# Kernel optimization log

Measured on AMD Instinct MI355X. Metric: run time of the kernel, lower is better.

Reference implementation:

```python
import jax, jax.numpy as jnp
import numpy as np

B, L, D, H, DH = 2, 2048, 1024, 16, 64
THETA_T = 100.0
EPS_COS = 1e-6
EPS_NORM = 1e-6


def make_rope_tables(n_heads=H, d_head=DH, theta_t=THETA_T):
    dr = d_head // 12                      # 5 rotary freqs per head per axis
    n = n_heads * dr
    log_min, log_max = np.log(np.pi), np.log(10.0 * np.pi)
    f = np.exp(np.linspace(log_min, log_max, n + 1)[:-1])
    freqs = np.stack([f, f]).reshape(2, dr, n_heads).transpose(0, 2, 1)   # (2, H, dr)
    t_freqs = (theta_t ** (-np.arange(n, dtype=np.float64) / n)).reshape(dr, n_heads).T  # (H, dr)
    return jnp.asarray(freqs, jnp.float32), jnp.asarray(t_freqs, jnp.float32)


def rms_norm(x, scale, eps=EPS_NORM):
    ms = jnp.mean(x.astype(jnp.float32) ** 2, axis=-1, keepdims=True)
    return x * (scale.astype(jnp.float32) * jax.lax.rsqrt(ms + eps)).astype(x.dtype)


def rope_theta(pos, pos_orig, time, freqs, t_freqs):
    # pos_to_use: (b, l, c=2, xy=2), mapped to [-1, 1]
    pos_use = jnp.stack([pos_orig, pos], axis=2) * 2.0 - 1.0
    theta_w = pos_use[..., 0][:, :, :, None, None] * freqs[0]      # b l 2 H dr
    theta_h = pos_use[..., 1][:, :, :, None, None] * freqs[1]      # b l 2 H dr
    theta_t = time[:, :, None, None, None] * t_freqs               # b l 1 H dr
    theta = jnp.concatenate([theta_h, theta_w, theta_t], axis=2)   # b l 5 H dr
    b, l = theta.shape[0], theta.shape[1]
    theta = jnp.transpose(theta, (0, 1, 3, 2, 4)).reshape(b, l, H, -1)  # b l H (5*dr)
    return theta


def apply_rotary_emb(x, theta):
    d = theta.shape[-1]
    x1, x2, x3 = x[..., :d], x[..., d:2 * d], x[..., 2 * d:]
    cos, sin = jnp.cos(theta), jnp.sin(theta)
    y1 = x1 * cos - x2 * sin
    y2 = x2 * cos + x1 * sin
    return jnp.concatenate([y1, y2, x3], axis=-1)


def scale_for_cosine_sim(q, k, scale, eps=EPS_COS):
    sq = jnp.sum(q * q, axis=-1, keepdims=True)
    sk = jnp.sum(k * k, axis=-1, keepdims=True)
    sqrt_scale = jnp.sqrt(scale)                         # (H,1,1) -> broadcasts to (b,H,l,1)
    return q * (sqrt_scale * jax.lax.rsqrt(sq + eps)), k * (sqrt_scale * jax.lax.rsqrt(sk + eps))


def setup_inputs() -> dict:
    key = jax.random.key(0)
    ks = jax.random.split(key, 8)
    return {
        "x": jax.random.normal(ks[0], (B, L, D), jnp.float32),
        "pos": jax.random.uniform(ks[1], (B, L, 2), jnp.float32),
        "pos_orig": jax.random.uniform(ks[2], (B, L, 2), jnp.float32),
        "time": jax.random.uniform(ks[3], (B, L), jnp.float32),
        "w_qkv": jax.random.normal(ks[4], (3 * D, D), jnp.float32) * (D ** -0.5),
        "w_out": jax.random.normal(ks[5], (D, D), jnp.float32) * (D ** -0.5),
        "w_up": jax.random.normal(ks[6], (4 * D, D), jnp.float32) * (D ** -0.5),
        "w_down": jax.random.normal(ks[7], (D, 4 * D), jnp.float32) * ((4 * D) ** -0.5),
        "norm1_scale": jnp.ones((D,), jnp.float32),
        "norm2_scale": jnp.ones((D,), jnp.float32),
        "qk_scale": jnp.full((H, 1, 1), 10.0, jnp.float32),
    }


def reference(x, pos, pos_orig, time, w_qkv, w_out, w_up, w_down,
              norm1_scale, norm2_scale, qk_scale):
    freqs, t_freqs = make_rope_tables()
    b, l, _ = x.shape

    # --- attention block (pre-norm) ---
    xn = rms_norm(x, norm1_scale)
    qkv = jnp.einsum('bld,ed->ble', xn, w_qkv)                  # b l 3D
    q, k, v = jnp.split(qkv, 3, axis=-1)
    q = q.reshape(b, l, H, DH)
    k = k.reshape(b, l, H, DH)
    v = v.reshape(b, l, H, DH).transpose(0, 2, 1, 3)            # b H l dh

    theta = rope_theta(pos, pos_orig, time, freqs, t_freqs)      # b l H 25
    q = apply_rotary_emb(q, theta).transpose(0, 2, 1, 3)         # b H l dh
    k = apply_rotary_emb(k, theta).transpose(0, 2, 1, 3)

    q, k = scale_for_cosine_sim(q, k, qk_scale)                  # cosine-sim QK norm
    scores = jnp.einsum('bhqd,bhkd->bhqk', q, k)                 # scale=1 (already folded in)
    probs = jax.nn.softmax(scores, axis=-1)
    attn = jnp.einsum('bhqk,bhkd->bhqd', probs, v)
    attn = attn.transpose(0, 2, 1, 3).reshape(b, l, D)
    x = x + jnp.einsum('bld,ed->ble', attn, w_out)

    h = rms_norm(x, norm2_scale)
    h = jax.nn.gelu(jnp.einsum('bld,ed->ble', h, w_up), approximate=True)
    x = x + jnp.einsum('ble,de->bld', h, w_down)
    return x
```

## Files before the change

kernel.cpp:

```cpp
#include <hip/hip_runtime.h>

#define B_ 2
#define L_ 2048
#define D_ 1024
#define H_ 16
#define DH_ 64

typedef float f32x4 __attribute__((ext_vector_type(4)));
typedef __bf16 bf16x8 __attribute__((ext_vector_type(8)));

__device__ __forceinline__ ushort f2bf(float f) {
  unsigned u = __float_as_uint(f);
  u += 0x7fffu + ((u >> 16) & 1u);
  return (ushort)(u >> 16);
}
__device__ __forceinline__ float bf2f(ushort h) {
  return __uint_as_float(((unsigned)h) << 16);
}

__device__ __forceinline__ void gload_lds16(const void* g, void* l) {
  __builtin_amdgcn_global_load_lds(
      (const __attribute__((address_space(1))) unsigned*)g,
      (__attribute__((address_space(3))) unsigned*)l, 16, 0, 0);
}

__device__ __forceinline__ float gelu_f(float v) {
  return 0.5f * v * (1.0f + tanhf(0.7978845608f * (v + 0.044715f * v * v * v)));
}

__global__ __launch_bounds__(256) void cast_all_kernel(const float* __restrict__ w0,
                                                       const float* __restrict__ w1,
                                                       const float* __restrict__ w2,
                                                       const float* __restrict__ w3,
                                                       ushort* __restrict__ o0,
                                                       ushort* __restrict__ o1,
                                                       ushort* __restrict__ o2,
                                                       ushort* __restrict__ o3) {
  int i = blockIdx.x * 256 + threadIdx.x;
  const float* src;
  ushort* dst;
  int j = i;
  if (j < 786432) { src = w0; dst = o0; }
  else if (j < 786432 + 262144) { j -= 786432; src = w1; dst = o1; }
  else if (j < 786432 + 262144 + 1048576) { j -= 786432 + 262144; src = w2; dst = o2; }
  else { j -= 786432 + 262144 + 1048576; src = w3; dst = o3; }
  float4 v = ((const float4*)src)[j];
  ushort4 o;
  o.x = f2bf(v.x); o.y = f2bf(v.y); o.z = f2bf(v.z); o.w = f2bf(v.w);
  ((ushort4*)dst)[j] = o;
}

template <typename T>
__global__ __launch_bounds__(256) void rmsnorm_kernel(const T* __restrict__ x,
                                                      const float* __restrict__ scale,
                                                      ushort* __restrict__ out) {
  int row = blockIdx.x, t = threadIdx.x;
  float4 v;
  if constexpr (sizeof(T) == 4) {
    v = ((const float4*)((const float*)x + (size_t)row * D_))[t];
  } else {
    ushort4 u = ((const ushort4*)((const ushort*)x + (size_t)row * D_))[t];
    v.x = bf2f(u.x); v.y = bf2f(u.y); v.z = bf2f(u.z); v.w = bf2f(u.w);
  }
  float ss = v.x * v.x + v.y * v.y + v.z * v.z + v.w * v.w;
#pragma unroll
  for (int d = 1; d < 64; d <<= 1) ss += __shfl_xor(ss, d);
  __shared__ float wsum[4];
  if ((t & 63) == 0) wsum[t >> 6] = ss;
  __syncthreads();
  float tot = wsum[0] + wsum[1] + wsum[2] + wsum[3];
  float r = rsqrtf(tot * (1.0f / D_) + 1e-6f);
  float4 sc = ((const float4*)scale)[t];
  ushort4 o;
  o.x = f2bf(v.x * sc.x * r); o.y = f2bf(v.y * sc.y * r);
  o.z = f2bf(v.z * sc.z * r); o.w = f2bf(v.w * sc.w * r);
  ((ushort4*)(out + (size_t)row * D_))[t] = o;
}

template <int EPI, int XR, int XC>
__global__ __launch_bounds__(512, 2) void gemm256(const ushort* __restrict__ A,
                                                  const ushort* __restrict__ Bw,
                                                  void* __restrict__ Cout,
                                                  int M, int N, int K) {
  __shared__ __align__(16) ushort Als[2][2][128 * 64];
  __shared__ __align__(16) ushort Bls[2][2][128 * 64];
  const int tid = threadIdx.x;
  const int lane = tid & 63;
  const int w = tid >> 6;
  const int wm = w >> 2, wn = w & 3;
  const int fr = lane & 15, fg = lane >> 4;
  const int bid = blockIdx.y * gridDim.x + blockIdx.x;
  const int xcd = bid & 7, i0 = bid >> 3;
  const int CR = gridDim.x / XR, CC = gridDim.y / XC;
  const int rt = (xcd % XR) * CR + (i0 % CR);
  const int ct = (xcd / XR) * CC + (i0 / CR);
  const int row0 = rt * 256, col0 = ct * 256;
  const ushort* Ab = A + (size_t)row0 * K;
  const ushort* Bb = Bw + (size_t)col0 * K;
  const int srow = tid >> 3;
  const int sxor = ((tid & 7) ^ (srow & 7)) * 8;

  f32x4 acc[8][4];
  f32x4 zero = {0.f, 0.f, 0.f, 0.f};
#pragma unroll
  for (int m = 0; m < 8; m++)
#pragma unroll
    for (int n = 0; n < 4; n++) acc[m][n] = zero;

  auto stageA = [&](int buf, int half, int kt) {
#pragma unroll
    for (int i = 0; i < 2; i++)
      gload_lds16(Ab + (size_t)(half * 128 + i * 64 + srow) * K + kt + sxor,
                  &Als[buf][half][i * 4096 + tid * 8]);
  };
  auto stageB = [&](int buf, int half, int kt) {
#pragma unroll
    for (int i = 0; i < 2; i++)
      gload_lds16(Bb + (size_t)(half * 128 + i * 64 + srow) * K + kt + sxor,
                  &Bls[buf][half][i * 4096 + tid * 8]);
  };
  const int nt = K >> 6;
  stageA(0, 0, 0); stageB(0, 0, 0); stageB(0, 1, 0); stageA(0, 1, 0);
  asm volatile("s_waitcnt vmcnt(0)" ::: "memory");
  __builtin_amdgcn_s_barrier();

  bf16x8 afr[4][2], b0[2][2], b1[2][2];
  for (int t = 0; t < nt; t++) {
    const int cur = t & 1, nxt = cur ^ 1;
    const int kn = (t + 1) << 6;
    const bool more = (t + 1 < nt);
#pragma unroll
    for (int mf = 0; mf < 4; mf++)
#pragma unroll
      for (int ks = 0; ks < 2; ks++) {
        int r = wm * 64 + mf * 16 + fr;
        afr[mf][ks] = *(const bf16x8*)&Als[cur][0][r * 64 + (((ks * 4 + fg) ^ (r & 7)) << 3)];
      }
#pragma unroll
    for (int nf = 0; nf < 2; nf++)
#pragma unroll
      for (int ks = 0; ks < 2; ks++) {
        int c = wn * 32 + nf * 16 + fr;
        b0[nf][ks] = *(const bf16x8*)&Bls[cur][0][c * 64 + (((ks * 4 + fg) ^ (c & 7)) << 3)];
      }
    if (more) stageA(nxt, 0, kn);
    asm volatile("s_waitcnt vmcnt(4)" ::: "memory");
    __builtin_amdgcn_s_barrier();
    asm volatile("s_waitcnt lgkmcnt(0)" ::: "memory");
    __builtin_amdgcn_sched_barrier(0);
    __builtin_amdgcn_s_setprio(1);
#pragma unroll
    for (int mf = 0; mf < 4; mf++)
#pragma unroll
      for (int nf = 0; nf < 2; nf++)
#pragma unroll
        for (int ks = 0; ks < 2; ks++)
          acc[mf][nf] =
              __builtin_amdgcn_mfma_f32_16x16x32_bf16(afr[mf][ks], b0[nf][ks], acc[mf][nf], 0, 0, 0);
    __builtin_amdgcn_s_setprio(0);
    __builtin_amdgcn_s_barrier();
#pragma unroll
    for (int nf = 0; nf < 2; nf++)
#pragma unroll
      for (int ks = 0; ks < 2; ks++) {
        int c = wn * 32 + nf * 16 + fr;
        b1[nf][ks] = *(const bf16x8*)&Bls[cur][1][c * 64 + (((ks * 4 + fg) ^ (c & 7)) << 3)];
      }
    if (more) stageB(nxt, 0, kn);
    asm volatile("s_waitcnt vmcnt(4)" ::: "memory");
    __builtin_amdgcn_s_barrier();
    asm volatile("s_waitcnt lgkmcnt(0)" ::: "memory");
    __builtin_amdgcn_sched_barrier(0);
    __builtin_amdgcn_s_setprio(1);
#pragma unroll
    for (int mf = 0; mf < 4; mf++)
#pragma unroll
      for (int nf = 0; nf < 2; nf++)
#pragma unroll
        for (int ks = 0; ks < 2; ks++)
          acc[mf][2 + nf] =
              __builtin_amdgcn_mfma_f32_16x16x32_bf16(afr[mf][ks], b1[nf][ks], acc[mf][2 + nf], 0, 0, 0);
    __builtin_amdgcn_s_setprio(0);
    __builtin_amdgcn_s_barrier();
#pragma unroll
    for (int mf = 0; mf < 4; mf++)
#pragma unroll
      for (int ks = 0; ks < 2; ks++) {
        int r = wm * 64 + mf * 16 + fr;
        afr[mf][ks] = *(const bf16x8*)&Als[cur][1][r * 64 + (((ks * 4 + fg) ^ (r & 7)) << 3)];
      }
    if (more) stageB(nxt, 1, kn);
    asm volatile("s_waitcnt vmcnt(4)" ::: "memory");
    __builtin_amdgcn_s_barrier();
    asm volatile("s_waitcnt lgkmcnt(0)" ::: "memory");
    __builtin_amdgcn_sched_barrier(0);
    __builtin_amdgcn_s_setprio(1);
#pragma unroll
    for (int mf = 0; mf < 4; mf++)
#pragma unroll
      for (int nf = 0; nf < 2; nf++)
#pragma unroll
        for (int ks = 0; ks < 2; ks++)
          acc[4 + mf][2 + nf] =
              __builtin_amdgcn_mfma_f32_16x16x32_bf16(afr[mf][ks], b1[nf][ks], acc[4 + mf][2 + nf], 0, 0, 0);
    __builtin_amdgcn_s_setprio(0);
    __builtin_amdgcn_s_barrier();
    if (more) stageA(nxt, 1, kn);
    asm volatile("s_waitcnt vmcnt(4)" ::: "memory");
    __builtin_amdgcn_s_barrier();
    asm volatile("s_waitcnt lgkmcnt(0)" ::: "memory");
    __builtin_amdgcn_sched_barrier(0);
    __builtin_amdgcn_s_setprio(1);
#pragma unroll
    for (int mf = 0; mf < 4; mf++)
#pragma unroll
      for (int nf = 0; nf < 2; nf++)
#pragma unroll
        for (int ks = 0; ks < 2; ks++)
          acc[4 + mf][nf] =
              __builtin_amdgcn_mfma_f32_16x16x32_bf16(afr[mf][ks], b0[nf][ks], acc[4 + mf][nf], 0, 0, 0);
    __builtin_amdgcn_s_setprio(0);
    __builtin_amdgcn_s_barrier();
  }
  const int orow = row0 + wm * 64 + fg * 4;
  const int ocol = col0 + wn * 32 + fr;
#pragma unroll
  for (int am = 0; am < 8; am++) {
#pragma unroll
    for (int j = 0; j < 4; j++) {
      int r = orow + (am >> 2) * 128 + (am & 3) * 16 + j;
#pragma unroll
      for (int an = 0; an < 4; an++) {
        int cidx = ocol + (an >> 1) * 128 + (an & 1) * 16;
        size_t idx = (size_t)r * N + cidx;
        float v = acc[am][an][j];
        if (EPI == 0) {
          ((ushort*)Cout)[idx] = f2bf(v);
        } else {
          ((ushort*)Cout)[idx] = f2bf(gelu_f(v));
        }
      }
    }
  }
}

template <int EPI, int BM, int BN, int DEPTH, int XR, int XC, bool CTFAST>
__global__ __launch_bounds__(256) void gemm_nt(const ushort* __restrict__ A,
                                               const ushort* __restrict__ Bw,
                                               void* __restrict__ Cout,
                                               const void* __restrict__ resid,
                                               int M, int N, int K, int Klen) {
  constexpr int WROWS = BM / 2, WCOLS = BN / 2;
  constexpr int MR = WROWS / 16, NR = WCOLS / 16;
  constexpr int ALOADS = BM / 64, BLOADS = BN / 64;
  constexpr int NLOADS = ALOADS + BLOADS;
  __shared__ __align__(16) ushort Als[DEPTH][BM * 32];
  __shared__ __align__(16) ushort Bls[DEPTH][BN * 32];
  const int tid = threadIdx.x;
  const int lane = tid & 63;
  const int w = tid >> 6;
  const int wr = w >> 1, wc = w & 1;
  const int bid = blockIdx.y * gridDim.x + blockIdx.x;
  const int xcd = bid & 7;
  const int i0 = bid >> 3;
  const int CR = gridDim.x / XR, CC = gridDim.y / XC;
  int rt, ct;
  if constexpr (CTFAST) {
    rt = (xcd % XR) * CR + (i0 / CC);
    ct = (xcd / XR) * CC + (i0 % CC);
  } else {
    rt = (xcd % XR) * CR + (i0 % CR);
    ct = (xcd / XR) * CC + (i0 / CR);
  }
  const int row0 = rt * BM;
  const int col0 = ct * BN;
  const int koff = blockIdx.z * Klen;
  const ushort* Ab = A + (size_t)row0 * K + koff;
  const ushort* Bb = Bw + (size_t)col0 * K + koff;
  const int sr = tid >> 2;
  const int scA = (((tid & 3) ^ ((tid >> 3) & 3)) * 8);
  const int fr = lane & 15;
  const int fg = lane >> 4;
  f32x4 zero = {0.f, 0.f, 0.f, 0.f};
  f32x4 acc[MR][NR];
#pragma unroll
  for (int m = 0; m < MR; m++)
#pragma unroll
    for (int n = 0; n < NR; n++) acc[m][n] = zero;

  auto stage = [&](int slot, int kt) {
#pragma unroll
    for (int i2 = 0; i2 < ALOADS; i2++)
      gload_lds16(Ab + (size_t)(sr + 64 * i2) * K + kt + scA, &Als[slot][i2 * 2048 + tid * 8]);
#pragma unroll
    for (int i2 = 0; i2 < BLOADS; i2++)
      gload_lds16(Bb + (size_t)(sr + 64 * i2) * K + kt + scA, &Bls[slot][i2 * 2048 + tid * 8]);
  };
  const int nt = Klen >> 5;
#pragma unroll
  for (int p = 0; p < DEPTH - 1; p++) stage(p, p << 5);
  int cur = 0, sbuf = DEPTH - 1;
  for (int t = 0; t < nt; t++) {
    const int ahead = nt - 1 - t;
    if constexpr (DEPTH == 3) {
      if (ahead >= 1) asm volatile("s_waitcnt vmcnt(%0)" ::"i"(NLOADS) : "memory");
      else            asm volatile("s_waitcnt vmcnt(0)" ::: "memory");
    } else if constexpr (DEPTH == 4) {
      if (ahead >= 2)      asm volatile("s_waitcnt vmcnt(%0)" ::"i"(2 * NLOADS) : "memory");
      else if (ahead == 1) asm volatile("s_waitcnt vmcnt(%0)" ::"i"(NLOADS) : "memory");
      else                 asm volatile("s_waitcnt vmcnt(0)" ::: "memory");
    } else {
      if (ahead >= 3)      asm volatile("s_waitcnt vmcnt(%0)" ::"i"(3 * NLOADS) : "memory");
      else if (ahead == 2) asm volatile("s_waitcnt vmcnt(%0)" ::"i"(2 * NLOADS) : "memory");
      else if (ahead == 1) asm volatile("s_waitcnt vmcnt(%0)" ::"i"(NLOADS) : "memory");
      else                 asm volatile("s_waitcnt vmcnt(0)" ::: "memory");
    }
    __builtin_amdgcn_s_barrier();
    if (t + DEPTH - 1 < nt) {
      stage(sbuf, (t + DEPTH - 1) << 5);
      sbuf = (sbuf == DEPTH - 1) ? 0 : sbuf + 1;
    }
    bf16x8 af[MR], bfr[NR];
#pragma unroll
    for (int m = 0; m < MR; m++) {
      int rA = wr * WROWS + m * 16 + fr;
      af[m] = *(const bf16x8*)&Als[cur][rA * 32 + ((fg ^ ((rA >> 1) & 3)) << 3)];
    }
#pragma unroll
    for (int n = 0; n < NR; n++) {
      int rB = wc * WCOLS + n * 16 + fr;
      bfr[n] = *(const bf16x8*)&Bls[cur][rB * 32 + ((fg ^ ((rB >> 1) & 3)) << 3)];
    }
#pragma unroll
    for (int m = 0; m < MR; m++)
#pragma unroll
      for (int n = 0; n < NR; n++)
        acc[m][n] = __builtin_amdgcn_mfma_f32_16x16x32_bf16(af[m], bfr[n], acc[m][n], 0, 0, 0);
    cur = (cur == DEPTH - 1) ? 0 : cur + 1;
  }
  const int orow = row0 + wr * WROWS + fg * 4;
  const int ocol = col0 + wc * WCOLS + fr;
  float* Pz = (float*)Cout + (size_t)blockIdx.z * M * N;
#pragma unroll
  for (int m = 0; m < MR; m++) {
#pragma unroll
    for (int j = 0; j < 4; j++) {
      int r = orow + m * 16 + j;
#pragma unroll
      for (int n = 0; n < NR; n++) {
        int cidx = ocol + n * 16;
        size_t idx = (size_t)r * N + cidx;
        float v = acc[m][n][j];
        if (EPI == 0) {
          ((ushort*)Cout)[idx] = f2bf(v);
        } else if (EPI == 1) {
          ((ushort*)Cout)[idx] = f2bf(((const float*)resid)[idx] + v);
        } else if (EPI == 2) {
          ((ushort*)Cout)[idx] = f2bf(gelu_f(v));
        } else if (EPI == 3) {
          ((float*)Cout)[idx] = bf2f(((const ushort*)resid)[idx]) + v;
        } else {
          Pz[idx] = v;
        }
      }
    }
  }
}

__global__ __launch_bounds__(256) void reduce_down_kernel(const float* __restrict__ P0,
                                                          const float* __restrict__ P1,
                                                          const ushort* __restrict__ residb,
                                                          float* __restrict__ out) {
  int i = blockIdx.x * 256 + threadIdx.x;
  float4 a = ((const float4*)P0)[i];
  float4 b = ((const float4*)P1)[i];
  ushort4 r = ((const ushort4*)residb)[i];
  float4 o;
  o.x = a.x + b.x + bf2f(r.x);
  o.y = a.y + b.y + bf2f(r.y);
  o.z = a.z + b.z + bf2f(r.z);
  o.w = a.w + b.w + bf2f(r.w);
  ((float4*)out)[i] = o;
}

__global__ __launch_bounds__(256) void rope_kernel(const ushort* __restrict__ qkv,
                                                   const float* __restrict__ pos,
                                                   const float* __restrict__ pos_orig,
                                                   const float* __restrict__ timep,
                                                   const float* __restrict__ qk_scale,
                                                   ushort* __restrict__ qr,
                                                   ushort* __restrict__ kr) {
  int gw = (blockIdx.x * 256 + threadIdx.x) >> 6;
  int lane = threadIdx.x & 63;
  int h = gw & 15;
  int row = gw >> 4;
  int b = row >> 11;
  int l = row & (L_ - 1);
  float qv = bf2f(qkv[(size_t)row * 3072 + h * 64 + lane]);
  float kv = bf2f(qkv[(size_t)row * 3072 + 1024 + h * 64 + lane]);
  float c = 1.0f, s = 0.0f;
  if (lane < 50) {
    int idx = lane < 25 ? lane : lane - 25;
    int sg = idx / 5, d = idx % 5;
    int fi = d * 16 + h;
    float th;
    if (sg == 4) {
      th = timep[row] * __expf(-(float)fi * 0.05756462732485115f);
    } else {
      float fr = 3.14159265358979323846f * __expf((float)fi * 0.028782313662425575f);
      const float* psrc = (sg == 0 || sg == 2) ? pos_orig : pos;
      int comp = (sg < 2) ? 1 : 0;
      th = (2.0f * psrc[(size_t)row * 2 + comp] - 1.0f) * fr;
    }
    s = sinf(th);
    c = cosf(th);
  }
  int partner = lane < 25 ? lane + 25 : lane - 25;
  float qp = __shfl(qv, partner, 64);
  float kp = __shfl(kv, partner, 64);
  float yq, yk;
  if (lane < 25) { yq = qv * c - qp * s; yk = kv * c - kp * s; }
  else if (lane < 50) { yq = qv * c + qp * s; yk = kv * c + kp * s; }
  else { yq = qv; yk = kv; }
  float sq = yq * yq, sk = yk * yk;
#pragma unroll
  for (int d = 1; d < 64; d <<= 1) { sq += __shfl_xor(sq, d); sk += __shfl_xor(sk, d); }
  float scl = sqrtf(qk_scale[h]);
  float qo = yq * scl * rsqrtf(sq + 1e-6f);
  float ko = yk * scl * rsqrtf(sk + 1e-6f);
  size_t o = ((size_t)(b * 16 + h) * L_ + l) * 64 + lane;
  qr[o] = f2bf(qo);
  kr[o] = f2bf(ko);
}

__global__ __launch_bounds__(256) void vtrans_kernel(const ushort* __restrict__ qkv,
                                                     ushort* __restrict__ vT) {
  __shared__ __align__(16) ushort tile[64][72];
  int t = threadIdx.x;
  int lt = blockIdx.x;
  int bh = blockIdx.y;
  int b = bh >> 4, h = bh & 15;
  int r = t >> 3, c0 = (t & 7) * 8;
#pragma unroll
  for (int half = 0; half < 2; half++) {
    const ushort* src =
        qkv + (size_t)(b * L_ + lt * 64 + r + half * 32) * 3072 + 2048 + h * 64 + c0;
    *(uint4*)&tile[r + half * 32][c0] = *(const uint4*)src;
  }
  __syncthreads();
#pragma unroll
  for (int half = 0; half < 2; half++) {
    int dh = r + half * 32;
    unsigned p0 = (unsigned)tile[c0 + 0][dh] | ((unsigned)tile[c0 + 1][dh] << 16);
    unsigned p1 = (unsigned)tile[c0 + 2][dh] | ((unsigned)tile[c0 + 3][dh] << 16);
    unsigned p2 = (unsigned)tile[c0 + 4][dh] | ((unsigned)tile[c0 + 5][dh] << 16);
    unsigned p3 = (unsigned)tile[c0 + 6][dh] | ((unsigned)tile[c0 + 7][dh] << 16);
    uint4 o; o.x = p0; o.y = p1; o.z = p2; o.w = p3;
    *(uint4*)&vT[((size_t)bh * 64 + dh) * L_ + lt * 64 + c0] = o;
  }
}

__global__ __launch_bounds__(256) void attn_kernel(const ushort* __restrict__ qr,
                                                   const ushort* __restrict__ kr,
                                                   const ushort* __restrict__ vT,
                                                   ushort* __restrict__ attnb) {
  __shared__ __align__(16) ushort Kls[2][64 * 64];
  __shared__ __align__(16) ushort Vls[2][64 * 64];
  __shared__ __align__(16) ushort Pls[4][2][16 * 64];
  const int tid = threadIdx.x, lane = tid & 63, w = tid >> 6;
  const int bid = blockIdx.x;
  const int qp = (bid >> 3) & 15;
  const int bh = (bid & 7) | ((bid >> 7) << 3);
  const int b = bh >> 4;
  const int fr = lane & 15, fg = lane >> 4;
  const ushort* Qb0 = qr + ((size_t)bh * L_ + qp * 128 + w * 16) * 64;
  const ushort* Qb1 = Qb0 + 64 * 64;
  bf16x8 qf0[2], qf1[2];
#pragma unroll
  for (int c = 0; c < 2; c++) {
    qf0[c] = *(const bf16x8*)(Qb0 + fr * 64 + c * 32 + fg * 8);
    qf1[c] = *(const bf16x8*)(Qb1 + fr * 64 + c * 32 + fg * 8);
  }
  const ushort ob[8] = {0x3F80, 0x3F80, 0x3F80, 0x3F80, 0x3F80, 0x3F80, 0x3F80, 0x3F80};
  const bf16x8 ones = *(const bf16x8*)ob;
  f32x4 zero = {0.f, 0.f, 0.f, 0.f};
  f32x4 accO0[4], accO1[4], acc1_0 = zero, acc1_1 = zero;
#pragma unroll
  for (int n = 0; n < 4; n++) { accO0[n] = zero; accO1[n] = zero; }
  const int sr = tid >> 3;
  const int scz = (((tid & 7) ^ (sr & 7)) * 8);
  auto stage = [&](int buf, int kt) {
    gload_lds16(kr + ((size_t)bh * L_ + kt + sr) * 64 + scz, &Kls[buf][tid * 8]);
    gload_lds16(kr + ((size_t)bh * L_ + kt + 32 + sr) * 64 + scz, &Kls[buf][2048 + tid * 8]);
    gload_lds16(vT + ((size_t)bh * 64 + sr) * L_ + kt + scz, &Vls[buf][tid * 8]);
    gload_lds16(vT + ((size_t)bh * 64 + 32 + sr) * L_ + kt + scz, &Vls[buf][2048 + tid * 8]);
  };
  stage(0, 0);
  int cur = 0;
  for (int t = 0; t < (L_ >> 6); t++) {
    asm volatile("s_waitcnt vmcnt(0)" ::: "memory");
    __builtin_amdgcn_s_barrier();
    __builtin_amdgcn_sched_barrier(0);
    if (t + 1 < (L_ >> 6)) stage(cur ^ 1, (t + 1) << 6);
    f32x4 sv0[4], sv1[4];
#pragma unroll
    for (int n = 0; n < 4; n++) { sv0[n] = zero; sv1[n] = zero; }
    __builtin_amdgcn_s_setprio(1);
#pragma unroll
    for (int c = 0; c < 2; c++) {
#pragma unroll
      for (int n = 0; n < 4; n++) {
        bf16x8 kf =
            *(const bf16x8*)&Kls[cur][(n * 16 + fr) * 64 + (((c * 4 + fg) ^ (fr & 7)) << 3)];
        sv0[n] = __builtin_amdgcn_mfma_f32_16x16x32_bf16(qf0[c], kf, sv0[n], 0, 0, 0);
        sv1[n] = __builtin_amdgcn_mfma_f32_16x16x32_bf16(qf1[c], kf, sv1[n], 0, 0, 0);
      }
    }
    __builtin_amdgcn_s_setprio(0);
#pragma unroll
    for (int qs = 0; qs < 2; qs++) {
      const f32x4* sv = qs ? sv1 : sv0;
#pragma unroll
      for (int j = 0; j < 4; j++) {
        int row = fg * 4 + j;
        int rbase = row * 64;
        int rx = row & 7;
#pragma unroll
        for (int n = 0; n < 4; n++) {
          float p = __builtin_amdgcn_exp2f(
              fmaf(sv[n][j], 1.4426950408889634f, -17.31234049066756f));
          int chunk = 2 * n + (fr >> 3);
          Pls[w][qs][rbase + ((chunk ^ rx) << 3) + (fr & 7)] =
              (ushort)(__float_as_uint(p) >> 16);
        }
      }
    }
    __builtin_amdgcn_s_setprio(1);
#pragma unroll
    for (int c = 0; c < 2; c++) {
      bf16x8 pa0 = *(const bf16x8*)&Pls[w][0][fr * 64 + (((c * 4 + fg) ^ (fr & 7)) << 3)];
      bf16x8 pa1 = *(const bf16x8*)&Pls[w][1][fr * 64 + (((c * 4 + fg) ^ (fr & 7)) << 3)];
#pragma unroll
      for (int n = 0; n < 4; n++) {
        bf16x8 vb =
            *(const bf16x8*)&Vls[cur][(n * 16 + fr) * 64 + (((c * 4 + fg) ^ (fr & 7)) << 3)];
        accO0[n] = __builtin_amdgcn_mfma_f32_16x16x32_bf16(pa0, vb, accO0[n], 0, 0, 0);
        accO1[n] = __builtin_amdgcn_mfma_f32_16x16x32_bf16(pa1, vb, accO1[n], 0, 0, 0);
      }
      acc1_0 = __builtin_amdgcn_mfma_f32_16x16x32_bf16(pa0, ones, acc1_0, 0, 0, 0);
      acc1_1 = __builtin_amdgcn_mfma_f32_16x16x32_bf16(pa1, ones, acc1_1, 0, 0, 0);
    }
    __builtin_amdgcn_s_setprio(0);
    cur ^= 1;
  }
#pragma unroll
  for (int qs = 0; qs < 2; qs++) {
    const f32x4* accO = qs ? accO1 : accO0;
    const f32x4& acc1 = qs ? acc1_1 : acc1_0;
    float inv[4];
#pragma unroll
    for (int j = 0; j < 4; j++) inv[j] = 1.0f / acc1[j];
#pragma unroll
    for (int n = 0; n < 4; n++) {
#pragma unroll
      for (int j = 0; j < 4; j++) {
        float o = accO[n][j] * inv[j];
        int qrow = qp * 128 + qs * 64 + w * 16 + fg * 4 + j;
        int dh = fr + n * 16;
        attnb[(size_t)(b * L_ + qrow) * 1024 + (bh & 15) * 64 + dh] = f2bf(o);
      }
    }
  }
}

extern "C" void kernel_launch(void* const* d_in, const int* in_sizes, int n_in,
                              void* d_out, int out_size, void* d_ws, size_t ws_size,
                              hipStream_t stream) {
  const float* x = (const float*)d_in[0];
  const float* pos = (const float*)d_in[1];
  const float* pos_orig = (const float*)d_in[2];
  const float* timep = (const float*)d_in[3];
  const float* w_qkv = (const float*)d_in[4];
  const float* w_out = (const float*)d_in[5];
  const float* w_up = (const float*)d_in[6];
  const float* w_down = (const float*)d_in[7];
  const float* norm1 = (const float*)d_in[8];
  const float* norm2 = (const float*)d_in[9];
  const float* qk_scale = (const float*)d_in[10];
  float* out = (float*)d_out;
  char* ws = (char*)d_ws;
  size_t off = 0;
  auto alloc = [&](size_t bytes) {
    void* p = ws + off;
    off += bytes;
    return p;
  };
  ushort* xn = (ushort*)alloc(8ull << 20);
  ushort* qkvb = (ushort*)alloc(32ull << 20);
  ushort* qrb = (ushort*)alloc(8ull << 20);
  ushort* krb = (ushort*)alloc(8ull << 20);
  ushort* vTb = (ushort*)alloc(8ull << 20);
  ushort* attnb = (ushort*)alloc(8ull << 20);
  ushort* x1b = (ushort*)alloc(8ull << 20);
  ushort* wqkvb = (ushort*)alloc(6ull << 20);
  ushort* woutb = (ushort*)alloc(2ull << 20);
  ushort* wupb = (ushort*)alloc(8ull << 20);
  ushort* wdownb = (ushort*)alloc(8ull << 20);
  float* Ppart = (float*)qrb;

  cast_all_kernel<<<12288, 256, 0, stream>>>(w_qkv, w_out, w_up, w_down,
                                             wqkvb, woutb, wupb, wdownb);

  rmsnorm_kernel<float><<<4096, 256, 0, stream>>>(x, norm1, xn);
  gemm256<0, 4, 2><<<dim3(16, 12), 512, 0, stream>>>(xn, wqkvb, qkvb, 4096, 3072, 1024);
  rope_kernel<<<16384, 256, 0, stream>>>(qkvb, pos, pos_orig, timep, qk_scale, qrb, krb);
  vtrans_kernel<<<dim3(32, 32), 256, 0, stream>>>(qkvb, vTb);
  attn_kernel<<<512, 256, 0, stream>>>(qrb, krb, vTb, attnb);
  gemm_nt<1, 64, 64, 5, 4, 2, false><<<dim3(64, 16), 256, 0, stream>>>(
      attnb, woutb, x1b, x, 4096, 1024, 1024, 1024);
  rmsnorm_kernel<ushort><<<4096, 256, 0, stream>>>(x1b, norm2, xn);
  gemm256<2, 4, 2><<<dim3(16, 16), 512, 0, stream>>>(xn, wupb, qkvb, 4096, 4096, 1024);
  gemm_nt<4, 128, 128, 4, 4, 2, true><<<dim3(32, 8, 2), 256, 0, stream>>>(
      qkvb, wdownb, Ppart, nullptr, 4096, 1024, 4096, 2048);
  reduce_down_kernel<<<4096, 256, 0, stream>>>(Ppart, Ppart + (4u << 20), x1b, out);
}
```

Baseline: 266.9 us.

## Split attention over two KV halves with a separate combine kernel

The attention kernel now launches twice as many blocks. Each block processes half of the key/value sequence and writes unnormalized fp32 partial outputs and softmax denominators to scratch buffers. A new combine kernel sums the two halves, normalizes, and casts to bf16. The log2(e) factor is folded into the q scaling in the rope kernel, and the constant max offset is dropped, so the inner loop does a bare exp2. The intent is better CU occupancy, at the cost of extra fp32 scratch traffic and another launch.

```diff
diff --git a/kernel.cpp b/kernel.cpp
--- a/kernel.cpp
+++ b/kernel.cpp
@@ -426,7 +426,7 @@
 #pragma unroll
   for (int d = 1; d < 64; d <<= 1) { sq += __shfl_xor(sq, d); sk += __shfl_xor(sk, d); }
   float scl = sqrtf(qk_scale[h]);
-  float qo = yq * scl * rsqrtf(sq + 1e-6f);
+  float qo = yq * (scl * 1.4426950408889634f) * rsqrtf(sq + 1e-6f);
   float ko = yk * scl * rsqrtf(sk + 1e-6f);
   size_t o = ((size_t)(b * 16 + h) * L_ + l) * 64 + lane;
   qr[o] = f2bf(qo);
@@ -463,14 +463,16 @@
 __global__ __launch_bounds__(256) void attn_kernel(const ushort* __restrict__ qr,
                                                    const ushort* __restrict__ kr,
                                                    const ushort* __restrict__ vT,
-                                                   ushort* __restrict__ attnb) {
+                                                   float* __restrict__ po,
+                                                   float* __restrict__ den) {
   __shared__ __align__(16) ushort Kls[2][64 * 64];
   __shared__ __align__(16) ushort Vls[2][64 * 64];
   __shared__ __align__(16) ushort Pls[4][2][16 * 64];
   const int tid = threadIdx.x, lane = tid & 63, w = tid >> 6;
   const int bid = blockIdx.x;
-  const int qp = (bid >> 3) & 15;
-  const int bh = (bid & 7) | ((bid >> 7) << 3);
+  const int kvh = (bid >> 3) & 1;
+  const int qp = (bid >> 4) & 15;
+  const int bh = (bid & 7) | ((bid >> 8) << 3);
   const int b = bh >> 4;
   const int fr = lane & 15, fg = lane >> 4;
   const ushort* Qb0 = qr + ((size_t)bh * L_ + qp * 128 + w * 16) * 64;
@@ -495,13 +497,14 @@
     gload_lds16(vT + ((size_t)bh * 64 + sr) * L_ + kt + scz, &Vls[buf][tid * 8]);
     gload_lds16(vT + ((size_t)bh * 64 + 32 + sr) * L_ + kt + scz, &Vls[buf][2048 + tid * 8]);
   };
-  stage(0, 0);
+  const int t0 = kvh << 4;
+  stage(0, t0 << 6);
   int cur = 0;
-  for (int t = 0; t < (L_ >> 6); t++) {
+  for (int t = t0; t < t0 + 16; t++) {
     asm volatile("s_waitcnt vmcnt(0)" ::: "memory");
     __builtin_amdgcn_s_barrier();
     __builtin_amdgcn_sched_barrier(0);
-    if (t + 1 < (L_ >> 6)) stage(cur ^ 1, (t + 1) << 6);
+    if (t + 1 < t0 + 16) stage(cur ^ 1, (t + 1) << 6);
     f32x4 sv0[4], sv1[4];
 #pragma unroll
     for (int n = 0; n < 4; n++) { sv0[n] = zero; sv1[n] = zero; }
@@ -527,8 +530,7 @@
         int rx = row & 7;
 #pragma unroll
         for (int n = 0; n < 4; n++) {
-          float p = __builtin_amdgcn_exp2f(
-              fmaf(sv[n][j], 1.4426950408889634f, -17.31234049066756f));
+          float p = __builtin_amdgcn_exp2f(sv[n][j]);
           int chunk = 2 * n + (fr >> 3);
           Pls[w][qs][rbase + ((chunk ^ rx) << 3) + (fr & 7)] =
               (ushort)(__float_as_uint(p) >> 16);
@@ -557,20 +559,44 @@
   for (int qs = 0; qs < 2; qs++) {
     const f32x4* accO = qs ? accO1 : accO0;
     const f32x4& acc1 = qs ? acc1_1 : acc1_0;
-    float inv[4];
-#pragma unroll
-    for (int j = 0; j < 4; j++) inv[j] = 1.0f / acc1[j];
+    int qbase = qp * 128 + qs * 64 + w * 16 + fg * 4;
+    if (fr == 0) {
+#pragma unroll
+      for (int j = 0; j < 4; j++)
+        den[(size_t)kvh * 65536 + bh * 2048 + qbase + j] = acc1[j];
+    }
 #pragma unroll
     for (int n = 0; n < 4; n++) {
 #pragma unroll
       for (int j = 0; j < 4; j++) {
-        float o = accO[n][j] * inv[j];
-        int qrow = qp * 128 + qs * 64 + w * 16 + fg * 4 + j;
+        int qrow = qbase + j;
         int dh = fr + n * 16;
-        attnb[(size_t)(b * L_ + qrow) * 1024 + (bh & 15) * 64 + dh] = f2bf(o);
-      }
-    }
-  }
+        po[(size_t)kvh * 4194304 + (size_t)(b * L_ + qrow) * 1024 + (bh & 15) * 64 + dh] =
+            accO[n][j];
+      }
+    }
+  }
+}
+
+__global__ __launch_bounds__(256) void attn_combine_kernel(const float* __restrict__ po,
+                                                           const float* __restrict__ den,
+                                                           ushort* __restrict__ attnb) {
+  int i = blockIdx.x * 256 + threadIdx.x;
+  int col4 = i & 255;
+  int row = i >> 8;
+  int h = col4 >> 4;
+  int b = row >> 11;
+  int qrow = row & 2047;
+  int bh = b * 16 + h;
+  float4 p0 = ((const float4*)po)[i];
+  float4 p1 = ((const float4*)(po + 4194304))[i];
+  float inv = 1.0f / (den[bh * 2048 + qrow] + den[65536 + bh * 2048 + qrow]);
+  ushort4 o;
+  o.x = f2bf((p0.x + p1.x) * inv);
+  o.y = f2bf((p0.y + p1.y) * inv);
+  o.z = f2bf((p0.z + p1.z) * inv);
+  o.w = f2bf((p0.w + p1.w) * inv);
+  ((ushort4*)attnb)[i] = o;
 }
 
 extern "C" void kernel_launch(void* const* d_in, const int* in_sizes, int n_in,
@@ -607,6 +633,8 @@
   ushort* wupb = (ushort*)alloc(8ull << 20);
   ushort* wdownb = (ushort*)alloc(8ull << 20);
   float* Ppart = (float*)qrb;
+  float* po = (float*)qkvb;
+  float* den = (float*)x1b;
 
   cast_all_kernel<<<12288, 256, 0, stream>>>(w_qkv, w_out, w_up, w_down,
                                              wqkvb, woutb, wupb, wdownb);
@@ -615,7 +643,8 @@
   gemm256<0, 4, 2><<<dim3(16, 12), 512, 0, stream>>>(xn, wqkvb, qkvb, 4096, 3072, 1024);
   rope_kernel<<<16384, 256, 0, stream>>>(qkvb, pos, pos_orig, timep, qk_scale, qrb, krb);
   vtrans_kernel<<<dim3(32, 32), 256, 0, stream>>>(qkvb, vTb);
-  attn_kernel<<<512, 256, 0, stream>>>(qrb, krb, vTb, attnb);
+  attn_kernel<<<1024, 256, 0, stream>>>(qrb, krb, vTb, po, den);
+  attn_combine_kernel<<<4096, 256, 0, stream>>>(po, den, attnb);
   gemm_nt<1, 64, 64, 5, 4, 2, false><<<dim3(64, 16), 256, 0, stream>>>(
       attnb, woutb, x1b, x, 4096, 1024, 1024, 1024);
   rmsnorm_kernel<ushort><<<4096, 256, 0, stream>>>(x1b, norm2, xn);
```

After: 273.2 us. 2.4% more time.
